# Kernel tuning notes

Measured on AMD Instinct MI355X. Metric: run time of the kernel, lower is better.

The kernel has to match this reference:

```python
import math
import jax, jax.numpy as jnp
import numpy as np

L, B, S, D, HID, NH = 4, 2, 2048, 1024, 1024, 16
C = HID // NH  # 64


def setup_inputs() -> dict:
    key = jax.random.key(0)
    ks = jax.random.split(key, 8)
    p = lambda k, shape: jax.random.normal(k, shape, jnp.float32) * 0.02
    return {
        "x": jax.random.normal(ks[0], (B, S, D), jnp.float32),
        "Wq": p(ks[1], (L, D, HID)), "bq": jnp.zeros((L, HID), jnp.float32),
        "Wk": p(ks[2], (L, D, HID)), "bk": jnp.zeros((L, HID), jnp.float32),
        "Wv": p(ks[3], (L, D, HID)), "bv": jnp.zeros((L, HID), jnp.float32),
        "Wo": p(ks[4], (L, HID, D)), "bo": jnp.zeros((L, D), jnp.float32),
        "W1": p(ks[5], (L, D, HID)), "b1": jnp.zeros((L, HID), jnp.float32),
        "W2": p(ks[6], (L, HID, D)), "b2": jnp.zeros((L, D), jnp.float32),
        "gamma": jnp.ones((L, D), jnp.float32),   # single LayerNorm reused twice per block
        "beta": jnp.zeros((L, D), jnp.float32),
    }


def _pos_enc(seq_len, d, n=1000.0):
    col = jnp.arange(seq_len, dtype=jnp.float32)[:, None]        # [S,1]
    row = jnp.arange(d)                                          # [D]
    exp = (2.0 * (row // 2).astype(jnp.float32)) / d
    mat = col / jnp.power(n, exp)[None, :]                       # [S,D]
    return jnp.where(row % 2 == 0, jnp.sin(mat), jnp.cos(mat))


def _layernorm(x, g, b, eps=1e-5):
    mu = jnp.mean(x, axis=-1, keepdims=True)
    var = jnp.mean((x - mu) ** 2, axis=-1, keepdims=True)        # biased, as torch
    return (x - mu) / jnp.sqrt(var + eps) * g + b


def _block(x, Wq, bq, Wk, bk, Wv, bv, Wo, bo, W1, b1, W2, b2, g, be):
    b_, s_, _ = x.shape
    q = ((x @ Wq + bq)).reshape(b_, s_, NH, C) / math.sqrt(C)
    k = (x @ Wk + bk).reshape(b_, s_, NH, C)
    v = (x @ Wv + bv).reshape(b_, s_, NH, C)
    # NOTE: faithful to original einsum '...hq,...hk->...hqk' -> per-token
    # attention over the CHANNEL axis c, with a (c,c) causal mask.
    aff = jnp.einsum('bshq,bshk->bshqk', q, k)                   # [B,S,H,C,C]
    mask = jnp.triu(jnp.ones((C, C), bool), 1)
    aff = jnp.where(mask, -jnp.inf, aff)
    w = jax.nn.softmax(aff, axis=-1)
    av = jnp.einsum('bshqk,bshk->bshq', w, v).reshape(b_, s_, HID)
    attn_out = av @ Wo + bo
    x = _layernorm(attn_out + x, g, be)
    mlp_out = jax.nn.relu(x @ W1 + b1) @ W2 + b2
    return _layernorm(mlp_out + x, g, be)


def reference(x, Wq, bq, Wk, bk, Wv, bv, Wo, bo, W1, b1, W2, b2, gamma, beta):
    x = x + _pos_enc(x.shape[1], x.shape[2])
    for i in range(L):
        x = _block(x, Wq[i], bq[i], Wk[i], bk[i], Wv[i], bv[i], Wo[i], bo[i],
                   W1[i], b1[i], W2[i], b2[i], gamma[i], beta[i])
    return x
```

## Files before the change

### kernel.cpp

```cpp
#include <hip/hip_runtime.h>
#include <hip/hip_bf16.h>
#include <stdint.h>

#define TOK 4096
#define DM  1024

using u16 = unsigned short;
typedef __attribute__((ext_vector_type(8))) short short8;
typedef __attribute__((ext_vector_type(4))) float f32x4;

__device__ __forceinline__ u16 f2bf(float f){
  unsigned u = __float_as_uint(f);
  return (u16)((u + 0x7fffu + ((u >> 16) & 1u)) >> 16);
}
__device__ __forceinline__ float bf2f(u16 h){ return __uint_as_float(((unsigned)h) << 16); }

__device__ __forceinline__ float fexp2(float x){
#if __has_builtin(__builtin_amdgcn_exp2f)
  return __builtin_amdgcn_exp2f(x);
#else
  float r; asm("v_exp_f32 %0, %1\n\ts_nop 0" : "=v"(r) : "v"(x)); return r;
#endif
}
__device__ __forceinline__ float frcp(float x){
#if __has_builtin(__builtin_amdgcn_rcpf)
  return __builtin_amdgcn_rcpf(x);
#else
  float r; asm("v_rcp_f32 %0, %1\n\ts_nop 0" : "=v"(r) : "v"(x)); return r;
#endif
}

__global__ __launch_bounds__(256) void posenc_add(
    const float* __restrict__ x, float* __restrict__ r, u16* __restrict__ xb)
{
  const int t = blockIdx.x;
  const int s = t & 2047;
  const size_t base = (size_t)t * DM;
#pragma unroll
  for (int i = 0; i < 4; ++i){
    const int d = threadIdx.x + i * 256;
    const float e = (float)(d & ~1) * (1.0f / (float)DM);
    const float denom = powf(1000.0f, e);
    const float mat = (float)s / denom;
    const float pe = (d & 1) ? cosf(mat) : sinf(mat);
    const float v = x[base + d] + pe;
    r[base + d] = v;
    xb[base + d] = f2bf(v);
  }
}

__global__ __launch_bounds__(256) void transpose6(
    const float* __restrict__ Wq, const float* __restrict__ Wk, const float* __restrict__ Wv,
    const float* __restrict__ Wo, const float* __restrict__ W1, const float* __restrict__ W2,
    u16* __restrict__ WT, int l0)
{
  __shared__ float tile[32][33];
  const int bid = blockIdx.x;
  const int l  = l0 + bid / 6144;
  const int mm = (bid >> 10) % 6;
  const int t  = bid & 1023;
  const int tn = (t & 31) * 32;
  const int tk = (t >> 5) * 32;
  const float* src = (mm==0)?Wq:(mm==1)?Wk:(mm==2)?Wv:(mm==3)?Wo:(mm==4)?W1:W2;
  src += (size_t)l * 1048576;
  u16* dst = WT + ((size_t)(l - l0) * 6 + mm) * 1048576;
  const int tx = threadIdx.x & 31, ty = threadIdx.x >> 5;
#pragma unroll
  for (int i = 0; i < 4; ++i)
    tile[ty + i*8][tx] = src[(size_t)(tk + ty + i*8) * 1024 + tn + tx];
  __syncthreads();
#pragma unroll
  for (int i = 0; i < 4; ++i)
    dst[(size_t)(tn + ty + i*8) * 1024 + tk + tx] = f2bf(tile[tx][ty + i*8]);
}

#define BM 128
#define BK 64
#define KD 1024

#define QS 200

__global__ __launch_bounds__(512, 4) void qkv_attn(
    const u16* __restrict__ A, const u16* __restrict__ WTq,
    const float* __restrict__ bq, const float* __restrict__ bk, const float* __restrict__ bv,
    u16* __restrict__ av)
{
  __shared__ __align__(16) u16 lds[128 * QS];
  u16* sA = lds;
  u16* sB = lds + 8192;
  const int tid  = threadIdx.x;
  const int lane = tid & 63;
  const int wave = tid >> 6;
  const int nwg = gridDim.x;
  const int wg  = (blockIdx.x & 7) * (nwg >> 3) + (blockIdx.x >> 3);
  const int h   = wg & 15;
  const int t0  = (wg >> 4) * BM;

  const int srow  = lane >> 3;
  const int sslot = (lane & 7) ^ srow;
  const u16* gA = A + (size_t)(t0 + wave*16 + srow) * KD + sslot * 8;
  u16* lA = sA + (wave*2) * 512;
  const int c0 = wave * 3;
  const u16* gB0 = WTq + (size_t)((c0+0)>>3)*1048576 + (size_t)(h*64 + ((c0+0)&7)*8 + srow)*KD + sslot*8;
  const u16* gB1 = WTq + (size_t)((c0+1)>>3)*1048576 + (size_t)(h*64 + ((c0+1)&7)*8 + srow)*KD + sslot*8;
  const u16* gB2 = WTq + (size_t)((c0+2)>>3)*1048576 + (size_t)(h*64 + ((c0+2)&7)*8 + srow)*KD + sslot*8;
  u16* lB0 = sB + (c0+0) * 512;
  u16* lB1 = sB + (c0+1) * 512;
  u16* lB2 = sB + (c0+2) * 512;

  const int wr = wave >> 2;
  const int wc = wave & 3;
  f32x4 acc[4][3] = {};

  for (int kt = 0; kt < KD/BK; ++kt){
    const int k0 = kt * BK;
#pragma unroll
    for (int p = 0; p < 2; ++p)
      __builtin_amdgcn_global_load_lds(
          (const __attribute__((address_space(1))) void*)(gA + p*8*KD + k0),
          (__attribute__((address_space(3))) void*)(lA + p*512), 16, 0, 0);
    __builtin_amdgcn_global_load_lds(
        (const __attribute__((address_space(1))) void*)(gB0 + k0),
        (__attribute__((address_space(3))) void*)lB0, 16, 0, 0);
    __builtin_amdgcn_global_load_lds(
        (const __attribute__((address_space(1))) void*)(gB1 + k0),
        (__attribute__((address_space(3))) void*)lB1, 16, 0, 0);
    __builtin_amdgcn_global_load_lds(
        (const __attribute__((address_space(1))) void*)(gB2 + k0),
        (__attribute__((address_space(3))) void*)lB2, 16, 0, 0);
    __syncthreads();
#pragma unroll
    for (int kk = 0; kk < 2; ++kk){
      short8 af[4], bfr[3];
      const int kidx = kk*4 + (lane >> 4);
#pragma unroll
      for (int i = 0; i < 4; ++i){
        const int arow = wr*64 + i*16 + (lane & 15);
        af[i] = *(const short8*)(sA + arow*64 + (kidx ^ (arow & 7)) * 8);
      }
#pragma unroll
      for (int j = 0; j < 3; ++j){
        const int brow = wc*48 + j*16 + (lane & 15);
        bfr[j] = *(const short8*)(sB + brow*64 + (kidx ^ (brow & 7)) * 8);
      }
#pragma unroll
      for (int i = 0; i < 4; ++i)
#pragma unroll
        for (int j = 0; j < 3; ++j)
          acc[i][j] = __builtin_amdgcn_mfma_f32_16x16x32_bf16(af[i], bfr[j], acc[i][j], 0, 0, 0);
    }
    __syncthreads();
  }

#pragma unroll
  for (int i = 0; i < 4; ++i){
    const int row = wr*64 + i*16 + (lane >> 4) * 4;
#pragma unroll
    for (int j = 0; j < 3; ++j){
      const int col = wc*48 + j*16 + (lane & 15);
      float bias;
      if (col < 64)       bias = bq[h*64 + col];
      else if (col < 128) bias = bk[h*64 + col - 64];
      else                bias = bv[h*64 + col - 128];
      const bool isq = (col < 64);
#pragma unroll
      for (int r = 0; r < 4; ++r){
        float v = acc[i][j][r] + bias;
        if (isq) v *= 0.125f;
        lds[(row + r) * QS + col] = f2bf(v);
      }
    }
  }
  __syncthreads();

  const int r3 = lane & 3;
  for (int tt = 0; tt < 16; tt += 2){
    const int ta = wave*16 + tt;
    const u16* rowa = lds + ta * QS;
    const u16* rowb = rowa + QS;
    const float qa = bf2f(rowa[lane]) * 1.44269504f;
    const float qb = bf2f(rowb[lane]) * 1.44269504f;
    float sa = 0.f, aa = 0.f, sb = 0.f, ab = 0.f;
#pragma unroll
    for (int j0 = 0; j0 < 64; j0 += 8){
      const short8 ka = *(const short8*)(rowa + 64 + j0);
      const short8 va = *(const short8*)(rowa + 128 + j0);
      const short8 kb = *(const short8*)(rowb + 64 + j0);
      const short8 vb = *(const short8*)(rowb + 128 + j0);
      const float bias0 = (j0 + 3 <= lane) ? 0.0f : -200.0f;
      const float bias1 = (j0 + 7 <= lane) ? 0.0f : -200.0f;
#pragma unroll
      for (int q = 0; q < 8; ++q){
        const float bias = (q < 4) ? bias0 : bias1;
        const float ea = fexp2(fmaf(qa, bf2f((u16)ka[q]), bias));
        const float eb = fexp2(fmaf(qb, bf2f((u16)kb[q]), bias));
        sa += ea; aa = fmaf(ea, bf2f((u16)va[q]), aa);
        sb += eb; ab = fmaf(eb, bf2f((u16)vb[q]), ab);
      }
    }
#pragma unroll
    for (int s = 0; s < 3; ++s){
      const int jj = lane - r3 + s;
      const float bias = (s <= r3 && r3 < 3) ? 0.0f : -200.0f;
      const float ea = fexp2(fmaf(qa, bf2f(rowa[64 + jj]), bias));
      const float eb = fexp2(fmaf(qb, bf2f(rowb[64 + jj]), bias));
      sa += ea; aa = fmaf(ea, bf2f(rowa[128 + jj]), aa);
      sb += eb; ab = fmaf(eb, bf2f(rowb[128 + jj]), ab);
    }
    av[(size_t)(t0 + ta)     * DM + h*64 + lane] = f2bf(aa * frcp(sa));
    av[(size_t)(t0 + ta + 1) * DM + h*64 + lane] = f2bf(ab * frcp(sb));
  }
}

template<int MODE, int BNt>
__global__ __launch_bounds__(256) void gemm_k1024(
    const u16* __restrict__ A, const u16* __restrict__ BT,
    const float* __restrict__ bias0,
    u16* __restrict__ outB, int M, int N)
{
  constexpr int NFR = BNt / 32;
  __shared__ __align__(16) u16 sA[BM*BK];
  __shared__ __align__(16) u16 sB[BNt*BK];
  const int tid  = threadIdx.x;
  const int lane = tid & 63;
  const int wave = tid >> 6;
  const int nbn = N / BNt;
  const int nwg = gridDim.x;
  const int wg  = (blockIdx.x & 7) * (nwg >> 3) + (blockIdx.x >> 3);
  const size_t m0 = (size_t)(wg / nbn) * BM;
  const size_t n0 = (size_t)(wg % nbn) * BNt;

  const int srow  = lane >> 3;
  const int sslot = (lane & 7) ^ srow;
  const u16* gA = A  + (m0 + wave*32 + srow) * KD + sslot * 8;
  const u16* gB = BT + (n0 + wave*(BNt/4) + srow) * KD + sslot * 8;
  u16* lA = sA + (wave*32) * 64;
  u16* lB = sB + (wave*(BNt/4)) * 64;

  const int wm = (wave >> 1) * 64;
  const int wn = (wave & 1) * (BNt/2);
  f32x4 acc[4][NFR] = {};

  for (int kt = 0; kt < KD/BK; ++kt){
    const int k0 = kt * BK;
#pragma unroll
    for (int p = 0; p < 4; ++p)
      __builtin_amdgcn_global_load_lds(
          (const __attribute__((address_space(1))) void*)(gA + p*8*KD + k0),
          (__attribute__((address_space(3))) void*)(lA + p*8*64), 16, 0, 0);
#pragma unroll
    for (int p = 0; p < BNt/32; ++p)
      __builtin_amdgcn_global_load_lds(
          (const __attribute__((address_space(1))) void*)(gB + p*8*KD + k0),
          (__attribute__((address_space(3))) void*)(lB + p*8*64), 16, 0, 0);
    __syncthreads();
#pragma unroll
    for (int kk = 0; kk < 2; ++kk){
      short8 af[4], bfr[NFR];
      const int kidx = kk*4 + (lane >> 4);
#pragma unroll
      for (int i = 0; i < 4; ++i){
        const int arow = wm + i*16 + (lane & 15);
        af[i]  = *(const short8*)(sA + arow*64 + (kidx ^ (arow & 7)) * 8);
      }
#pragma unroll
      for (int j = 0; j < NFR; ++j){
        const int brow = wn + j*16 + (lane & 15);
        bfr[j] = *(const short8*)(sB + brow*64 + (kidx ^ (brow & 7)) * 8);
      }
#pragma unroll
      for (int i = 0; i < 4; ++i)
#pragma unroll
        for (int j = 0; j < NFR; ++j)
          acc[i][j] = __builtin_amdgcn_mfma_f32_16x16x32_bf16(af[i], bfr[j], acc[i][j], 0, 0, 0);
    }
    __syncthreads();
  }

#pragma unroll
  for (int i = 0; i < 4; ++i){
    const int growb = wm + i*16 + (lane >> 4) * 4;
#pragma unroll
    for (int j = 0; j < NFR; ++j){
      const size_t gcol = n0 + wn + j*16 + (lane & 15);
      const float bv = bias0[gcol];
#pragma unroll
      for (int r = 0; r < 4; ++r){
        const size_t grow = m0 + growb + r;
        float v = acc[i][j][r] + bv;
        if constexpr (MODE == 1) v = fmaxf(v, 0.0f);
        outB[grow * N + gcol] = f2bf(v);
      }
    }
  }
}

__global__ __launch_bounds__(256) void residual_ln(
    const u16* __restrict__ y, const float* xres,
    const float* __restrict__ gamma, const float* __restrict__ beta,
    float* xout, u16* __restrict__ xb)
{
  __shared__ float red[4];
  const int row = blockIdx.x, tid = threadIdx.x;
  const int lane = tid & 63, wave = tid >> 6;
  const ushort4 a = ((const ushort4*)(y + (size_t)row*DM))[tid];
  const float4  b = ((const float4*)(xres + (size_t)row*DM))[tid];
  float4 s; s.x=bf2f(a.x)+b.x; s.y=bf2f(a.y)+b.y; s.z=bf2f(a.z)+b.z; s.w=bf2f(a.w)+b.w;
  float p = s.x + s.y + s.z + s.w;
#pragma unroll
  for (int o = 32; o; o >>= 1) p += __shfl_xor(p, o);
  if (lane == 0) red[wave] = p;
  __syncthreads();
  const float mu = (red[0]+red[1]+red[2]+red[3]) * (1.0f/(float)DM);
  __syncthreads();
  const float dx=s.x-mu, dy=s.y-mu, dz=s.z-mu, dw=s.w-mu;
  float q2 = dx*dx + dy*dy + dz*dz + dw*dw;
#pragma unroll
  for (int o = 32; o; o >>= 1) q2 += __shfl_xor(q2, o);
  if (lane == 0) red[wave] = q2;
  __syncthreads();
  const float var = (red[0]+red[1]+red[2]+red[3]) * (1.0f/(float)DM);
  const float rstd = rsqrtf(var + 1e-5f);
  const float4 g  = ((const float4*)gamma)[tid];
  const float4 be = ((const float4*)beta)[tid];
  float4 o4;
  o4.x = dx*rstd*g.x + be.x;
  o4.y = dy*rstd*g.y + be.y;
  o4.z = dz*rstd*g.z + be.z;
  o4.w = dw*rstd*g.w + be.w;
  ((float4*)(xout + (size_t)row*DM))[tid] = o4;
  ushort4 ob; ob.x=f2bf(o4.x); ob.y=f2bf(o4.y); ob.z=f2bf(o4.z); ob.w=f2bf(o4.w);
  ((ushort4*)(xb + (size_t)row*DM))[tid] = ob;
}

extern "C" void kernel_launch(void* const* d_in, const int* in_sizes, int n_in,
                              void* d_out, int out_size, void* d_ws, size_t ws_size,
                              hipStream_t stream)
{
  const float* x    = (const float*)d_in[0];
  const float* Wq   = (const float*)d_in[1];
  const float* bq   = (const float*)d_in[2];
  const float* Wk   = (const float*)d_in[3];
  const float* bk   = (const float*)d_in[4];
  const float* Wv   = (const float*)d_in[5];
  const float* bv   = (const float*)d_in[6];
  const float* Wo   = (const float*)d_in[7];
  const float* bo   = (const float*)d_in[8];
  const float* W1   = (const float*)d_in[9];
  const float* b1   = (const float*)d_in[10];
  const float* W2   = (const float*)d_in[11];
  const float* b2   = (const float*)d_in[12];
  const float* gam  = (const float*)d_in[13];
  const float* bet  = (const float*)d_in[14];

  char* ws = (char*)d_ws;
  size_t off = 0;
  auto alloc = [&](size_t b){ void* p = ws + off; off = (off + b + 255) & ~(size_t)255; return p; };

  const size_t oneWT = 6ull*1048576*2;
  const size_t rest  = ((size_t)TOK*DM*4)
                     + ((size_t)TOK*DM*2)
                     + ((size_t)TOK*DM*2)
                     + ((size_t)TOK*DM*2)
                     + ((size_t)TOK*DM*2)
                     + 4096;
  const bool all4 = (4*oneWT + rest) <= ws_size;

  u16*   WT   = (u16*)  alloc(all4 ? 4*oneWT : oneWT);
  float* res  = (float*)alloc((size_t)TOK*DM*4);
  u16*   xb   = (u16*)  alloc((size_t)TOK*DM*2);
  u16*   avb  = (u16*)  alloc((size_t)TOK*DM*2);
  u16*   hbuf = (u16*)  alloc((size_t)TOK*DM*2);
  u16*   ybuf = (u16*)  alloc((size_t)TOK*DM*2);
  if (off > ws_size) return;

  posenc_add<<<TOK, 256, 0, stream>>>(x, res, xb);
  if (all4)
    transpose6<<<4*6*1024, 256, 0, stream>>>(Wq, Wk, Wv, Wo, W1, W2, WT, 0);

  for (int l = 0; l < 4; ++l){
    u16* wt = all4 ? (WT + (size_t)l * 6 * 1048576) : WT;
    if (!all4)
      transpose6<<<6*1024, 256, 0, stream>>>(Wq, Wk, Wv, Wo, W1, W2, WT, l);
    qkv_attn<<<(TOK/BM)*16, 512, 0, stream>>>(
        xb, wt, bq + l*1024, bk + l*1024, bv + l*1024, avb);
    gemm_k1024<0,64><<<(TOK/BM)*(1024/64), 256, 0, stream>>>(
        avb, wt + 3ull*1048576, bo + l*1024, ybuf, TOK, 1024);
    residual_ln<<<TOK, 256, 0, stream>>>(ybuf, res, gam + l*1024, bet + l*1024, res, xb);
    gemm_k1024<1,64><<<(TOK/BM)*(1024/64), 256, 0, stream>>>(
        xb, wt + 4ull*1048576, b1 + l*1024, hbuf, TOK, 1024);
    gemm_k1024<0,64><<<(TOK/BM)*(1024/64), 256, 0, stream>>>(
        hbuf, wt + 5ull*1048576, b2 + l*1024, ybuf, TOK, 1024);
    float* xdst = (l == 3) ? (float*)d_out : res;
    residual_ln<<<TOK, 256, 0, stream>>>(ybuf, res, gam + l*1024, bet + l*1024, xdst, xb);
  }
}
```

Measured before the change: 621.8 us.

## Double-buffer LDS staging in GEMMs and retile QKV-attention to 64-token blocks

Both the fused QKV+attention kernel and the generic K=1024 GEMM now keep two LDS buffers. The next K-tile's global-to-LDS loads are issued before computing the current tile, so each K step needs only one barrier and load latency can overlap with MFMA work. The QKV kernel is also retiled from 128 tokens with 512 threads to 64 tokens with 256 threads and a K step of 32. In that kernel one wave loads activations and three waves load weights. This doubles the grid and changes the LDS swizzle. The trade-off is more LDS per block, about 49KB in the GEMM, which may lower occupancy, plus more, smaller blocks in the attention kernel that reread the weight tiles more often.

```diff
diff --git a/kernel.cpp b/kernel.cpp
--- a/kernel.cpp
+++ b/kernel.cpp
@@ -80,84 +80,84 @@
 
 #define QS 200
 
-__global__ __launch_bounds__(512, 4) void qkv_attn(
+__global__ __launch_bounds__(256, 4) void qkv_attn(
     const u16* __restrict__ A, const u16* __restrict__ WTq,
     const float* __restrict__ bq, const float* __restrict__ bk, const float* __restrict__ bv,
     u16* __restrict__ av)
 {
-  __shared__ __align__(16) u16 lds[128 * QS];
-  u16* sA = lds;
-  u16* sB = lds + 8192;
+  __shared__ __align__(16) u16 lds[16384];
   const int tid  = threadIdx.x;
   const int lane = tid & 63;
   const int wave = tid >> 6;
   const int nwg = gridDim.x;
   const int wg  = (blockIdx.x & 7) * (nwg >> 3) + (blockIdx.x >> 3);
   const int h   = wg & 15;
-  const int t0  = (wg >> 4) * BM;
-
-  const int srow  = lane >> 3;
-  const int sslot = (lane & 7) ^ srow;
-  const u16* gA = A + (size_t)(t0 + wave*16 + srow) * KD + sslot * 8;
-  u16* lA = sA + (wave*2) * 512;
-  const int c0 = wave * 3;
-  const u16* gB0 = WTq + (size_t)((c0+0)>>3)*1048576 + (size_t)(h*64 + ((c0+0)&7)*8 + srow)*KD + sslot*8;
-  const u16* gB1 = WTq + (size_t)((c0+1)>>3)*1048576 + (size_t)(h*64 + ((c0+1)&7)*8 + srow)*KD + sslot*8;
-  const u16* gB2 = WTq + (size_t)((c0+2)>>3)*1048576 + (size_t)(h*64 + ((c0+2)&7)*8 + srow)*KD + sslot*8;
-  u16* lB0 = sB + (c0+0) * 512;
-  u16* lB1 = sB + (c0+1) * 512;
-  u16* lB2 = sB + (c0+2) * 512;
-
-  const int wr = wave >> 2;
-  const int wc = wave & 3;
+  const int t0  = (wg >> 4) * 64;
+
+  const int srow  = lane >> 2;
+  const int sslot = (lane & 3) ^ (srow & 3);
+  const u16* g[4]; int lo[4];
+#pragma unroll
+  for (int p = 0; p < 4; ++p){
+    if (wave == 0){
+      g[p]  = A + (size_t)(t0 + p*16 + srow) * KD + sslot * 8;
+      lo[p] = p * 512;
+    } else {
+      const int c = (wave - 1) * 4 + p;
+      const int m = c >> 2;
+      g[p]  = WTq + (size_t)m * 1048576
+            + (size_t)(h*64 + (c & 3) * 16 + srow) * KD + sslot * 8;
+      lo[p] = 2048 + c * 512;
+    }
+  }
+
   f32x4 acc[4][3] = {};
 
-  for (int kt = 0; kt < KD/BK; ++kt){
-    const int k0 = kt * BK;
-#pragma unroll
-    for (int p = 0; p < 2; ++p)
+  auto stage = [&](int kt, int buf){
+    u16* base = lds + buf * 8192;
+    const int k0 = kt * 32;
+#pragma unroll
+    for (int p = 0; p < 4; ++p)
       __builtin_amdgcn_global_load_lds(
-          (const __attribute__((address_space(1))) void*)(gA + p*8*KD + k0),
-          (__attribute__((address_space(3))) void*)(lA + p*512), 16, 0, 0);
-    __builtin_amdgcn_global_load_lds(
-        (const __attribute__((address_space(1))) void*)(gB0 + k0),
-        (__attribute__((address_space(3))) void*)lB0, 16, 0, 0);
-    __builtin_amdgcn_global_load_lds(
-        (const __attribute__((address_space(1))) void*)(gB1 + k0),
-        (__attribute__((address_space(3))) void*)lB1, 16, 0, 0);
-    __builtin_amdgcn_global_load_lds(
-        (const __attribute__((address_space(1))) void*)(gB2 + k0),
-        (__attribute__((address_space(3))) void*)lB2, 16, 0, 0);
+          (const __attribute__((address_space(1))) void*)(g[p] + k0),
+          (__attribute__((address_space(3))) void*)(base + lo[p]), 16, 0, 0);
+  };
+  auto compute = [&](int buf){
+    const u16* sAc = lds + buf * 8192;
+    const u16* sBc = sAc + 2048;
+    const int kg = lane >> 4;
+    short8 af[4], bfr[3];
+#pragma unroll
+    for (int i = 0; i < 4; ++i){
+      const int arow = i*16 + (lane & 15);
+      af[i] = *(const short8*)(sAc + arow*32 + (kg ^ (arow & 3)) * 8);
+    }
+#pragma unroll
+    for (int j = 0; j < 3; ++j){
+      const int brow = wave*48 + j*16 + (lane & 15);
+      bfr[j] = *(const short8*)(sBc + brow*32 + (kg ^ (brow & 3)) * 8);
+    }
+#pragma unroll
+    for (int i = 0; i < 4; ++i)
+#pragma unroll
+      for (int j = 0; j < 3; ++j)
+        acc[i][j] = __builtin_amdgcn_mfma_f32_16x16x32_bf16(af[i], bfr[j], acc[i][j], 0, 0, 0);
+  };
+
+  stage(0, 0);
+  __syncthreads();
+  for (int kt = 0; kt < 32; ++kt){
+    if (kt + 1 < 32) stage(kt + 1, (kt + 1) & 1);
+    compute(kt & 1);
     __syncthreads();
-#pragma unroll
-    for (int kk = 0; kk < 2; ++kk){
-      short8 af[4], bfr[3];
-      const int kidx = kk*4 + (lane >> 4);
-#pragma unroll
-      for (int i = 0; i < 4; ++i){
-        const int arow = wr*64 + i*16 + (lane & 15);
-        af[i] = *(const short8*)(sA + arow*64 + (kidx ^ (arow & 7)) * 8);
-      }
-#pragma unroll
-      for (int j = 0; j < 3; ++j){
-        const int brow = wc*48 + j*16 + (lane & 15);
-        bfr[j] = *(const short8*)(sB + brow*64 + (kidx ^ (brow & 7)) * 8);
-      }
-#pragma unroll
-      for (int i = 0; i < 4; ++i)
-#pragma unroll
-        for (int j = 0; j < 3; ++j)
-          acc[i][j] = __builtin_amdgcn_mfma_f32_16x16x32_bf16(af[i], bfr[j], acc[i][j], 0, 0, 0);
-    }
-    __syncthreads();
   }
 
 #pragma unroll
   for (int i = 0; i < 4; ++i){
-    const int row = wr*64 + i*16 + (lane >> 4) * 4;
+    const int row = i*16 + (lane >> 4) * 4;
 #pragma unroll
     for (int j = 0; j < 3; ++j){
-      const int col = wc*48 + j*16 + (lane & 15);
+      const int col = wave*48 + j*16 + (lane & 15);
       float bias;
       if (col < 64)       bias = bq[h*64 + col];
       else if (col < 128) bias = bk[h*64 + col - 64];
@@ -213,14 +213,13 @@
 }
 
 template<int MODE, int BNt>
-__global__ __launch_bounds__(256) void gemm_k1024(
+__global__ __launch_bounds__(256, 2) void gemm_k1024(
     const u16* __restrict__ A, const u16* __restrict__ BT,
     const float* __restrict__ bias0,
     u16* __restrict__ outB, int M, int N)
 {
   constexpr int NFR = BNt / 32;
-  __shared__ __align__(16) u16 sA[BM*BK];
-  __shared__ __align__(16) u16 sB[BNt*BK];
+  __shared__ __align__(16) u16 lds2[2][(BM + BNt) * BK];
   const int tid  = threadIdx.x;
   const int lane = tid & 63;
   const int wave = tid >> 6;
@@ -234,26 +233,30 @@
   const int sslot = (lane & 7) ^ srow;
   const u16* gA = A  + (m0 + wave*32 + srow) * KD + sslot * 8;
   const u16* gB = BT + (n0 + wave*(BNt/4) + srow) * KD + sslot * 8;
-  u16* lA = sA + (wave*32) * 64;
-  u16* lB = sB + (wave*(BNt/4)) * 64;
+  const int loA = (wave*32) * 64;
+  const int loB = BM*BK + (wave*(BNt/4)) * 64;
 
   const int wm = (wave >> 1) * 64;
   const int wn = (wave & 1) * (BNt/2);
   f32x4 acc[4][NFR] = {};
 
-  for (int kt = 0; kt < KD/BK; ++kt){
+  auto stage = [&](int kt, int buf){
+    u16* base = lds2[buf];
     const int k0 = kt * BK;
 #pragma unroll
     for (int p = 0; p < 4; ++p)
       __builtin_amdgcn_global_load_lds(
           (const __attribute__((address_space(1))) void*)(gA + p*8*KD + k0),
-          (__attribute__((address_space(3))) void*)(lA + p*8*64), 16, 0, 0);
+          (__attribute__((address_space(3))) void*)(base + loA + p*512), 16, 0, 0);
 #pragma unroll
     for (int p = 0; p < BNt/32; ++p)
       __builtin_amdgcn_global_load_lds(
           (const __attribute__((address_space(1))) void*)(gB + p*8*KD + k0),
-          (__attribute__((address_space(3))) void*)(lB + p*8*64), 16, 0, 0);
-    __syncthreads();
+          (__attribute__((address_space(3))) void*)(base + loB + p*512), 16, 0, 0);
+  };
+  auto compute = [&](int buf){
+    const u16* sAc = lds2[buf];
+    const u16* sBc = sAc + BM*BK;
 #pragma unroll
     for (int kk = 0; kk < 2; ++kk){
       short8 af[4], bfr[NFR];
@@ -261,12 +264,12 @@
 #pragma unroll
       for (int i = 0; i < 4; ++i){
         const int arow = wm + i*16 + (lane & 15);
-        af[i]  = *(const short8*)(sA + arow*64 + (kidx ^ (arow & 7)) * 8);
+        af[i]  = *(const short8*)(sAc + arow*64 + (kidx ^ (arow & 7)) * 8);
       }
 #pragma unroll
       for (int j = 0; j < NFR; ++j){
         const int brow = wn + j*16 + (lane & 15);
-        bfr[j] = *(const short8*)(sB + brow*64 + (kidx ^ (brow & 7)) * 8);
+        bfr[j] = *(const short8*)(sBc + brow*64 + (kidx ^ (brow & 7)) * 8);
       }
 #pragma unroll
       for (int i = 0; i < 4; ++i)
@@ -274,6 +277,13 @@
         for (int j = 0; j < NFR; ++j)
           acc[i][j] = __builtin_amdgcn_mfma_f32_16x16x32_bf16(af[i], bfr[j], acc[i][j], 0, 0, 0);
     }
+  };
+
+  stage(0, 0);
+  __syncthreads();
+  for (int kt = 0; kt < KD/BK; ++kt){
+    if (kt + 1 < KD/BK) stage(kt + 1, (kt + 1) & 1);
+    compute(kt & 1);
     __syncthreads();
   }
 
@@ -382,7 +392,7 @@
     u16* wt = all4 ? (WT + (size_t)l * 6 * 1048576) : WT;
     if (!all4)
       transpose6<<<6*1024, 256, 0, stream>>>(Wq, Wk, Wv, Wo, W1, W2, WT, l);
-    qkv_attn<<<(TOK/BM)*16, 512, 0, stream>>>(
+    qkv_attn<<<(TOK/64)*16, 256, 0, stream>>>(
         xb, wt, bq + l*1024, bk + l*1024, bv + l*1024, avb);
     gemm_k1024<0,64><<<(TOK/BM)*(1024/64), 256, 0, stream>>>(
         avb, wt + 3ull*1048576, bo + l*1024, ybuf, TOK, 1024);
```

After: 622.0 us. Within noise of the previous version (+0.0%).
